# Kernel tuning notes

Measured on AMD Instinct MI355X. Metric: run time of the kernel, lower is better.

Reference implementation:

```python
import jax, jax.numpy as jnp
import numpy as np

HIDDEN = 300
LN_EPS = 1e-5


def _pair_indices(L, K):
    # row-major (emo, cau) order matches torch cat/reshape in couple_generator
    i = np.arange(L)[:, None]
    j = np.arange(L)[None, :]
    mask = np.abs(j - i) <= K
    emo, cau = np.nonzero(mask)
    return emo.astype(np.int32), cau.astype(np.int32)


def setup_inputs() -> dict:
    key = jax.random.key(0)
    ks = jax.random.split(key, 10)
    B, L, D = 32, 128, HIDDEN
    K = 12
    pos_dim = 50
    inp = {
        "h_e": jax.random.normal(ks[0], (B, L, D), jnp.float32),
        "h_c": jax.random.normal(ks[1], (B, L, D), jnp.float32),
        "h_share": jax.random.normal(ks[2], (B, L, D), jnp.float32),
        "pos_emb": jax.random.normal(ks[3], (2 * K + 1, pos_dim), jnp.float32) * 0.1,
        "W_hid": jax.random.normal(ks[4], (D, 2 * D + pos_dim), jnp.float32) * 0.02,
        "b_hid": jnp.zeros((D,), jnp.float32),
        "ln_g": jnp.ones((D,), jnp.float32),
        "ln_b": jnp.zeros((D,), jnp.float32),
        "W_rel": jax.random.normal(ks[5], (1, D), jnp.float32) * 0.02,
        "b_rel": jnp.zeros((1,), jnp.float32),
        "K": K,
    }
    return inp


def reference(h_e, h_c, h_share, pos_emb, W_hid, b_hid, ln_g, ln_b, W_rel, b_rel, K):
    B, L, D = h_e.shape
    he = h_e + h_share
    hc = h_c + h_share
    emo, cau = _pair_indices(L, int(K))  # static index constants
    rel = (cau - emo).astype(np.float32)  # [n]
    rp = jnp.asarray(cau - emo + int(K), jnp.int32)  # shifted rel pos
    # gather-concat pair features: [B, n, 2D]
    couples = jnp.concatenate([he[:, emo, :], hc[:, cau, :]], axis=-1)
    # Gaussian kernel over relative positions: [n, n]
    rel_j = jnp.asarray(rel)
    kernel = jnp.exp(-jnp.square(rel_j[:, None] - rel_j[None, :]))
    # smooth position embeddings (batch-independent): [n, pos_dim]
    rel_pos_emb = kernel @ pos_emb[rp]
    pair = jnp.concatenate(
        [couples, jnp.broadcast_to(rel_pos_emb[None], (B,) + rel_pos_emb.shape)],
        axis=-1,
    )
    h = jnp.einsum("bnf,df->bnd", pair, W_hid) + b_hid
    mu = jnp.mean(h, axis=-1, keepdims=True)
    var = jnp.mean(jnp.square(h - mu), axis=-1, keepdims=True)
    h = (h - mu) * jax.lax.rsqrt(var + LN_EPS) * ln_g + ln_b
    h = jax.nn.elu(h)  # dropout is identity in eval mode
    out = jnp.einsum("bnd,od->bno", h, W_rel) + b_rel
    return out[..., 0]  # [B, n_couple]
```

## Files before the change

kernel.cpp:

```cpp
#include <hip/hip_runtime.h>
#include <hip/hip_bf16.h>
#include <math.h>

#define BB 32
#define LL 128
#define DD 300
#define PD 50
#define KW 12
#define NP 3044
#define FF 650
#define NR 25
#define KP 320
#define NPAD 320
#define MM 4096
#define LN_EPS 1e-5f

typedef __attribute__((ext_vector_type(8))) short short8;
typedef __attribute__((ext_vector_type(4))) float f32x4;
typedef __attribute__((ext_vector_type(4))) int i32x4;

__device__ __forceinline__ unsigned short f2b(float f) {
    union { float f; unsigned int u; } v; v.f = f;
    unsigned int u = v.u;
    unsigned int r = u + 0x7FFFu + ((u >> 16) & 1u);
    return (unsigned short)(r >> 16);
}

__device__ __forceinline__ int row_start(int i) {
    if (i <= 12) return i * 13 + (i * (i - 1)) / 2;
    if (i <= 116) return 222 + 25 * (i - 12);
    int s = i - 116;
    return 2822 + 24 * s - (s * (s - 1)) / 2;
}

#define PREP_W_BLOCKS 800

__global__ __launch_bounds__(256) void prep_kernel(
    const float* __restrict__ pos_emb, const float* __restrict__ W_hid,
    const float* __restrict__ b_hid, float* __restrict__ P,
    unsigned short* __restrict__ Wbf)
{
    const int tid = threadIdx.x;
    if (blockIdx.x < NR) {
        __shared__ float sm[PD];
        const int r = blockIdx.x;
        if (tid < PD) {
            float acc = 0.f;
            #pragma unroll
            for (int d = 0; d < NR; d++) {
                int ad = d - KW; if (ad < 0) ad = -ad;
                float cnt = (float)(LL - ad);
                float diff = (float)(r - d);
                acc += cnt * expf(-diff * diff) * pos_emb[d * PD + tid];
            }
            sm[tid] = acc;
        }
        __syncthreads();
        for (int dd = tid; dd < DD; dd += 256) {
            float a = b_hid[dd];
            const float* w = W_hid + dd * FF + 2 * DD;
            #pragma unroll
            for (int k = 0; k < PD; k++) a += sm[k] * w[k];
            P[r * DD + dd] = a;
        }
    } else {
        int idx = (blockIdx.x - NR) * 256 + tid;
        int z = idx / (NPAD * KP);
        int rem = idx - z * (NPAD * KP);
        int d = rem / KP;
        int k = rem - d * KP;
        unsigned short v = 0;
        if (d < DD && k < DD) v = f2b(W_hid[d * FF + z * DD + k]);
        Wbf[idx] = v;
    }
}

__global__ __launch_bounds__(256) void gemm_kernel(
    const float* __restrict__ h_e, const float* __restrict__ h_c,
    const float* __restrict__ h_share, const unsigned short* __restrict__ Wbf,
    float* __restrict__ E, float* __restrict__ Cc)
{
    __shared__ unsigned short Bs[160 * 40];

    const int z = blockIdx.z;
    const int m0 = blockIdx.x * 64;
    const int n0 = blockIdx.y * 160;
    const int tid = threadIdx.x;
    const int wid = tid >> 6;
    const int lane = tid & 63;
    const int nn = lane & 15;
    const int q  = lane >> 4;

    const int row = m0 + wid * 16 + nn;
    const float* xr = (z ? h_c : h_e) + (size_t)row * DD;
    const float* sr = h_share + (size_t)row * DD;
    const unsigned short* Wbase = Wbf + (size_t)(z * NPAD + n0) * KP;

    f32x4 acc[10];
    #pragma unroll
    for (int f = 0; f < 10; f++) acc[f] = (f32x4){0.f, 0.f, 0.f, 0.f};

    for (int k0 = 0; k0 < KP; k0 += 32) {
        for (int i = tid; i < 640; i += 256) {
            int n = i >> 2;
            int c = i & 3;
            i32x4 v = *(const i32x4*)&Wbase[n * KP + k0 + c * 8];
            *(i32x4*)&Bs[n * 40 + c * 8] = v;
        }
        __syncthreads();

        const int kb = k0 + q * 8;
        float a8[8];
        if (kb + 7 < DD) {
            float4 x0 = *(const float4*)&xr[kb];
            float4 x1 = *(const float4*)&xr[kb + 4];
            float4 s0 = *(const float4*)&sr[kb];
            float4 s1 = *(const float4*)&sr[kb + 4];
            a8[0] = x0.x + s0.x; a8[1] = x0.y + s0.y;
            a8[2] = x0.z + s0.z; a8[3] = x0.w + s0.w;
            a8[4] = x1.x + s1.x; a8[5] = x1.y + s1.y;
            a8[6] = x1.z + s1.z; a8[7] = x1.w + s1.w;
        } else {
            #pragma unroll
            for (int u = 0; u < 8; u++) {
                int k = kb + u;
                a8[u] = (k < DD) ? (xr[k] + sr[k]) : 0.f;
            }
        }
        short8 a;
        #pragma unroll
        for (int u = 0; u < 8; u++) a[u] = (short)f2b(a8[u]);

        #pragma unroll
        for (int f = 0; f < 10; f++) {
            short8 b = *(const short8*)&Bs[(f * 16 + nn) * 40 + q * 8];
            acc[f] = __builtin_amdgcn_mfma_f32_16x16x32_bf16(a, b, acc[f], 0, 0, 0);
        }
        __syncthreads();
    }

    float* O = z ? Cc : E;
    const int orow = m0 + wid * 16 + q * 4;
    #pragma unroll
    for (int f = 0; f < 10; f++) {
        int col = n0 + f * 16 + nn;
        if (col < DD) {
            #pragma unroll
            for (int r = 0; r < 4; r++)
                O[(size_t)(orow + r) * DD + col] = acc[f][r];
        }
    }
}

__global__ __launch_bounds__(256) void pair_kernel(
    const float* __restrict__ E, const float* __restrict__ Cc,
    const float* __restrict__ P, const float* __restrict__ ln_g,
    const float* __restrict__ ln_b, const float* __restrict__ W_rel,
    const float* __restrict__ b_rel, float* __restrict__ out)
{
    const int wid = threadIdx.x >> 6;
    const int lane = threadIdx.x & 63;
    const int slot = blockIdx.x;
    const int b = slot >> 7;
    const int i = slot & 127;

    const float* e_row = E + (size_t)(b * LL + i) * DD;

    float e[5], g[5], gb[5], wr[5];
    #pragma unroll
    for (int t = 0; t < 5; t++) {
        int d = lane + 64 * t;
        if (d < DD) {
            e[t]  = e_row[d];
            g[t]  = ln_g[d];
            gb[t] = ln_b[d];
            wr[t] = W_rel[d];
        } else {
            e[t] = 0.f; g[t] = 0.f; gb[t] = 0.f; wr[t] = 0.f;
        }
    }
    const float brel = b_rel[0];

    int jlo = i - KW; if (jlo < 0) jlo = 0;
    int jhi = i + KW; if (jhi > LL - 1) jhi = LL - 1;
    const int base = b * NP + row_start(i);

    for (int j = jlo + wid; j <= jhi; j += 4) {
        const float* c_row = Cc + (size_t)(b * LL + j) * DD;
        const float* p_row = P + (j - i + KW) * DD;

        float h[5];
        float s = 0.f, ss = 0.f;
        #pragma unroll
        for (int t = 0; t < 5; t++) {
            int d = lane + 64 * t;
            h[t] = 0.f;
            if (d < DD) {
                h[t] = e[t] + c_row[d] + p_row[d];
                s += h[t];
                ss += h[t] * h[t];
            }
        }
        #pragma unroll
        for (int m = 1; m < 64; m <<= 1) {
            s  += __shfl_xor(s, m, 64);
            ss += __shfl_xor(ss, m, 64);
        }
        const float mean = s * (1.f / (float)DD);
        float var = ss * (1.f / (float)DD) - mean * mean;
        if (var < 0.f) var = 0.f;
        const float rstd = rsqrtf(var + LN_EPS);

        float acc = 0.f;
        #pragma unroll
        for (int t = 0; t < 5; t++) {
            int d = lane + 64 * t;
            if (d < DD) {
                float y = (h[t] - mean) * rstd * g[t] + gb[t];
                float el = y > 0.f ? y : (__expf(y) - 1.f);
                acc += el * wr[t];
            }
        }
        #pragma unroll
        for (int m = 1; m < 64; m <<= 1) acc += __shfl_xor(acc, m, 64);

        if (lane == 0) out[base + (j - jlo)] = acc + brel;
    }
}

extern "C" void kernel_launch(void* const* d_in, const int* in_sizes, int n_in,
                              void* d_out, int out_size, void* d_ws, size_t ws_size,
                              hipStream_t stream) {
    const float* h_e     = (const float*)d_in[0];
    const float* h_c     = (const float*)d_in[1];
    const float* h_share = (const float*)d_in[2];
    const float* pos_emb = (const float*)d_in[3];
    const float* W_hid   = (const float*)d_in[4];
    const float* b_hid   = (const float*)d_in[5];
    const float* ln_g    = (const float*)d_in[6];
    const float* ln_b    = (const float*)d_in[7];
    const float* W_rel   = (const float*)d_in[8];
    const float* b_rel   = (const float*)d_in[9];

    float* out = (float*)d_out;

    float* ws = (float*)d_ws;
    float* E   = ws;
    float* C   = E + (size_t)MM * DD;
    float* P   = C + (size_t)MM * DD;
    unsigned short* Wbf = (unsigned short*)(P + NR * DD);

    prep_kernel<<<dim3(NR + PREP_W_BLOCKS), dim3(256), 0, stream>>>(
        pos_emb, W_hid, b_hid, P, Wbf);

    gemm_kernel<<<dim3(MM / 64, 2, 2), dim3(256), 0, stream>>>(
        h_e, h_c, h_share, Wbf, E, C);

    pair_kernel<<<dim3(BB * LL), dim3(256), 0, stream>>>(
        E, C, P, ln_g, ln_b, W_rel, b_rel, out);
}
```

Measured before the change: 131.4 us.

## Process four pairs per wavefront in pair kernel with 16-lane groups

The pair kernel now launches one 64-thread wave per (batch, emo row) instead of four waves. Each wave splits into four 16-lane groups, and each group handles one cause position, so every lane keeps 19 feature elements in registers. This shortens the shuffle reductions to 4 steps and cuts the per-block setup of loading the e, gamma, beta and W_rel rows from four waves to one. The LayerNorm affine step is folded into FMAs. In exchange, each lane holds far more registers and threads per block drop, which can lower latency hiding, and the last iteration leaves some groups idle when the window length is not a multiple of four.

```diff
diff --git a/kernel.cpp b/kernel.cpp
--- a/kernel.cpp
+++ b/kernel.cpp
@@ -152,32 +152,30 @@
     }
 }
 
-__global__ __launch_bounds__(256) void pair_kernel(
+__global__ __launch_bounds__(64) void pair_kernel(
     const float* __restrict__ E, const float* __restrict__ Cc,
     const float* __restrict__ P, const float* __restrict__ ln_g,
     const float* __restrict__ ln_b, const float* __restrict__ W_rel,
     const float* __restrict__ b_rel, float* __restrict__ out)
 {
-    const int wid = threadIdx.x >> 6;
-    const int lane = threadIdx.x & 63;
+    const int lane = threadIdx.x;
+    const int qd = lane >> 4;
+    const int l16 = lane & 15;
     const int slot = blockIdx.x;
     const int b = slot >> 7;
     const int i = slot & 127;
 
     const float* e_row = E + (size_t)(b * LL + i) * DD;
 
-    float e[5], g[5], gb[5], wr[5];
+    float e[19], g[19], gb[19], wr[19];
     #pragma unroll
-    for (int t = 0; t < 5; t++) {
-        int d = lane + 64 * t;
-        if (d < DD) {
-            e[t]  = e_row[d];
-            g[t]  = ln_g[d];
-            gb[t] = ln_b[d];
-            wr[t] = W_rel[d];
-        } else {
-            e[t] = 0.f; g[t] = 0.f; gb[t] = 0.f; wr[t] = 0.f;
-        }
+    for (int t = 0; t < 19; t++) {
+        int d = l16 + 16 * t;
+        bool v = d < DD;
+        e[t]  = v ? e_row[d] : 0.f;
+        g[t]  = v ? ln_g[d]  : 0.f;
+        gb[t] = v ? ln_b[d]  : 0.f;
+        wr[t] = v ? W_rel[d] : 0.f;
     }
     const float brel = b_rel[0];
 
@@ -185,24 +183,27 @@
     int jhi = i + KW; if (jhi > LL - 1) jhi = LL - 1;
     const int base = b * NP + row_start(i);
 
-    for (int j = jlo + wid; j <= jhi; j += 4) {
-        const float* c_row = Cc + (size_t)(b * LL + j) * DD;
-        const float* p_row = P + (j - i + KW) * DD;
-
-        float h[5];
+    for (int j0 = jlo; j0 <= jhi; j0 += 4) {
+        const int j = j0 + qd;
+        const int jc = (j <= jhi) ? j : jhi;
+        const float* c_row = Cc + (size_t)(b * LL + jc) * DD;
+        const float* p_row = P + (jc - i + KW) * DD;
+
+        float h[19];
         float s = 0.f, ss = 0.f;
         #pragma unroll
-        for (int t = 0; t < 5; t++) {
-            int d = lane + 64 * t;
-            h[t] = 0.f;
+        for (int t = 0; t < 19; t++) {
+            int d = l16 + 16 * t;
+            float hv = 0.f;
             if (d < DD) {
-                h[t] = e[t] + c_row[d] + p_row[d];
-                s += h[t];
-                ss += h[t] * h[t];
+                hv = e[t] + c_row[d] + p_row[d];
+                s += hv;
+                ss += hv * hv;
             }
-        }
-        #pragma unroll
-        for (int m = 1; m < 64; m <<= 1) {
+            h[t] = hv;
+        }
+        #pragma unroll
+        for (int m = 1; m < 16; m <<= 1) {
             s  += __shfl_xor(s, m, 64);
             ss += __shfl_xor(ss, m, 64);
         }
@@ -213,18 +214,17 @@
 
         float acc = 0.f;
         #pragma unroll
-        for (int t = 0; t < 5; t++) {
-            int d = lane + 64 * t;
-            if (d < DD) {
-                float y = (h[t] - mean) * rstd * g[t] + gb[t];
-                float el = y > 0.f ? y : (__expf(y) - 1.f);
-                acc += el * wr[t];
-            }
-        }
-        #pragma unroll
-        for (int m = 1; m < 64; m <<= 1) acc += __shfl_xor(acc, m, 64);
-
-        if (lane == 0) out[base + (j - jlo)] = acc + brel;
+        for (int t = 0; t < 19; t++) {
+            float A = rstd * g[t];
+            float Bc = __builtin_fmaf(-mean, A, gb[t]);
+            float y = __builtin_fmaf(h[t], A, Bc);
+            float el = y > 0.f ? y : (__expf(y) - 1.f);
+            acc = __builtin_fmaf(el, wr[t], acc);
+        }
+        #pragma unroll
+        for (int m = 1; m < 16; m <<= 1) acc += __shfl_xor(acc, m, 64);
+
+        if (l16 == 0 && j <= jhi) out[base + (j - jlo)] = acc + brel;
     }
 }
 
@@ -256,6 +256,6 @@
     gemm_kernel<<<dim3(MM / 64, 2, 2), dim3(256), 0, stream>>>(
         h_e, h_c, h_share, Wbf, E, C);
 
-    pair_kernel<<<dim3(BB * LL), dim3(256), 0, stream>>>(
+    pair_kernel<<<dim3(BB * LL), dim3(64), 0, stream>>>(
         E, C, P, ln_g, ln_b, W_rel, b_rel, out);
 }
```

Result: slower. 135.4 us (+3.1%).
